# Performance work log

Measured on AMD Instinct MI355X. Metric: run time of the kernel, lower is better.

The kernel has to match this reference:

```python
import jax, jax.numpy as jnp
import numpy as np

N_NODES = 100000
N_EDGES = 1600000
F_IN, NH1, NH2, NH3, N_CLS = 128, 64, 18, 9, 10
KS = [8, 6, 4, 4]
BN_EPS = 1e-5


def setup_inputs() -> dict:
    key = jax.random.key(0)
    ks = jax.random.split(key, 32)
    inp = {
        "x": jax.random.normal(ks[0], (N_NODES, F_IN), dtype=jnp.float32),
        "edge_index": jax.random.randint(ks[1], (2, N_EDGES), 0, N_NODES, dtype=jnp.int32),
    }
    dims = [(F_IN, NH1), (NH1, NH2), (NH2, NH3), (NH3, N_CLS)]
    for i, ((din, dout), K) in enumerate(zip(dims, KS), start=1):
        scale = 1.0 / np.sqrt(din * K)
        inp[f"W{i}"] = jax.random.normal(ks[2 * i], (K, din, dout), dtype=jnp.float32) * scale
        inp[f"b{i}"] = jnp.zeros((dout,), dtype=jnp.float32)
    for i, d in enumerate([NH1, NH2, NH3], start=1):
        inp[f"bn{i}_g"] = jnp.ones((d,), dtype=jnp.float32)
        inp[f"bn{i}_b"] = jnp.zeros((d,), dtype=jnp.float32)
        inp[f"bn{i}_m"] = jnp.zeros((d,), dtype=jnp.float32)
        inp[f"bn{i}_v"] = jnp.ones((d,), dtype=jnp.float32)
    return inp


def _cheb_conv(x, W, b, src, dst, w_norm, n_nodes):
    # PyG ChebConv with lambda_max=2: L_hat = -D^{-1/2} A D^{-1/2}
    def prop(t):  # L_hat @ t via edge scatter
        return jax.ops.segment_sum(w_norm[:, None] * t[src], dst, num_segments=n_nodes)

    K = W.shape[0]
    Tx0 = x
    out = Tx0 @ W[0]
    Tx1 = prop(Tx0)
    out = out + Tx1 @ W[1]
    for k in range(2, K):
        Tx2 = 2.0 * prop(Tx1) - Tx0
        out = out + Tx2 @ W[k]
        Tx0, Tx1 = Tx1, Tx2
    return out + b


def _bn_eval(x, g, b, m, v):
    return (x - m) * (g * jax.lax.rsqrt(v + BN_EPS)) + b


def reference(x, edge_index, W1, b1, W2, b2, W3, b3, W4, b4,
              bn1_g, bn1_b, bn1_m, bn1_v,
              bn2_g, bn2_b, bn2_m, bn2_v,
              bn3_g, bn3_b, bn3_m, bn3_v):
    n = x.shape[0]
    src, dst = edge_index[0], edge_index[1]
    ones = jnp.ones((src.shape[0],), dtype=x.dtype)
    deg = jax.ops.segment_sum(ones, dst, num_segments=n)
    dinv = jnp.where(deg > 0, jax.lax.rsqrt(jnp.maximum(deg, 1.0)), 0.0)
    w_norm = -dinv[src] * dinv[dst]

    h = jax.nn.relu(_bn_eval(_cheb_conv(x, W1, b1, src, dst, w_norm, n), bn1_g, bn1_b, bn1_m, bn1_v))
    h = jax.nn.relu(_bn_eval(_cheb_conv(h, W2, b2, src, dst, w_norm, n), bn2_g, bn2_b, bn2_m, bn2_v))
    h = jax.nn.relu(_bn_eval(_cheb_conv(h, W3, b3, src, dst, w_norm, n), bn3_g, bn3_b, bn3_m, bn3_v))
    return _cheb_conv(h, W4, b4, src, dst, w_norm, n)
```

## Files before the change

kernel.cpp:

```cpp
#include <hip/hip_runtime.h>

#define NN 100000
#define NE 1600000
#define BN_EPS 1e-5f

#define BSH 7
#define BSZ (1 << BSH)
#define NBUCK 782
#define NC 192
#define CE 8334

typedef _Float16 half1;
typedef _Float16 half4 __attribute__((ext_vector_type(4)));
typedef _Float16 h8 __attribute__((ext_vector_type(8)));
typedef float f4 __attribute__((ext_vector_type(4)));
typedef float f8 __attribute__((ext_vector_type(8)));

static inline int divup(int a, int b) { return (a + b - 1) / b; }

__device__ __forceinline__ float wsrc(unsigned int q) {
    unsigned int dg = q >> 17;
    return dg ? rsqrtf((float)dg) : 0.f;
}


__global__ void hist2_kernel(const int* __restrict__ dst, int* __restrict__ deg,
                             int* __restrict__ hist_g) {
    __shared__ int h[NBUCK];
    int c = blockIdx.x;
    for (int i = threadIdx.x; i < NBUCK; i += blockDim.x) h[i] = 0;
    __syncthreads();
    int e0 = c * CE, e1 = min(e0 + CE, NE);
    for (int e = e0 + threadIdx.x; e < e1; e += blockDim.x) {
        int d = dst[e];
        atomicAdd(&deg[d], 1);
        atomicAdd(&h[d >> BSH], 1);
    }
    __syncthreads();
    for (int i = threadIdx.x; i < NBUCK; i += blockDim.x) hist_g[c * NBUCK + i] = h[i];
}

__global__ void blksum_kernel(const int* __restrict__ deg, int* __restrict__ blk, int n) {
    __shared__ int red[256];
    int t = threadIdx.x;
    int base = blockIdx.x * 1024 + t * 4;
    int s = 0;
#pragma unroll
    for (int i = 0; i < 4; ++i) {
        int idx = base + i;
        if (idx < n) s += deg[idx];
    }
    red[t] = s;
    __syncthreads();
    for (int off = 128; off > 0; off >>= 1) {
        if (t < off) red[t] += red[t + off];
        __syncthreads();
    }
    if (t == 0) blk[blockIdx.x] = red[0];
}

__global__ void blkscan_kernel(int* __restrict__ blk, int nb, int* __restrict__ row_ptr, int n) {
    __shared__ int sh[256];
    int t = threadIdx.x;
    int v = (t < nb) ? blk[t] : 0;
    sh[t] = v;
    __syncthreads();
    for (int off = 1; off < 256; off <<= 1) {
        int u = (t >= off) ? sh[t - off] : 0;
        __syncthreads();
        sh[t] += u;
        __syncthreads();
    }
    if (t < nb) blk[t] = (t == 0) ? 0 : sh[t - 1];
    if (t == nb - 1) row_ptr[n] = sh[t];
}

__global__ void emit_kernel(const int* __restrict__ deg, const int* __restrict__ blk,
                            int* __restrict__ row_ptr, int n) {
    __shared__ int red[256];
    int t = threadIdx.x;
    int base = blockIdx.x * 1024 + t * 4;
    int d[4];
    int s = 0;
#pragma unroll
    for (int i = 0; i < 4; ++i) {
        int idx = base + i;
        d[i] = (idx < n) ? deg[idx] : 0;
        s += d[i];
    }
    red[t] = s;
    __syncthreads();
    for (int off = 1; off < 256; off <<= 1) {
        int u = (t >= off) ? red[t - off] : 0;
        __syncthreads();
        red[t] += u;
        __syncthreads();
    }
    int run = blk[blockIdx.x] + ((t == 0) ? 0 : red[t - 1]);
#pragma unroll
    for (int i = 0; i < 4; ++i) {
        int idx = base + i;
        if (idx < n) { row_ptr[idx] = run; run += d[i]; }
    }
}

__global__ void bucketoff_kernel(const int* __restrict__ row_ptr, const int* __restrict__ hist_g,
                                 int* __restrict__ off_g) {
    int b = blockIdx.x * blockDim.x + threadIdx.x;
    if (b >= NBUCK) return;
    int run = row_ptr[b << BSH];
#pragma unroll 4
    for (int c = 0; c < NC; ++c) {
        off_g[c * NBUCK + b] = run;
        run += hist_g[c * NBUCK + b];
    }
}

__global__ void binscatter_kernel(const int* __restrict__ src, const int* __restrict__ dst,
                                  const int* __restrict__ deg, const int* __restrict__ off_g,
                                  int2* __restrict__ tmp) {
    __shared__ int off_l[NBUCK];
    int myx = blockIdx.x & 7;
    int c = blockIdx.x >> 3;
    for (int i = threadIdx.x; i < NBUCK; i += blockDim.x)
        off_l[i] = ((i & 7) == myx) ? off_g[c * NBUCK + i] : 0;
    __syncthreads();
    int e0 = c * CE, e1 = min(e0 + CE, NE);
    for (int e = e0 + threadIdx.x; e < e1; e += blockDim.x) {
        int d = dst[e];
        int b = d >> BSH;
        if ((b & 7) != myx) continue;
        int s = src[e];
        int dg = deg[s];
        if (dg > 32767) dg = 32767;
        int pos = atomicAdd(&off_l[b], 1);
        tmp[pos] = make_int2(s | (dg << 17), d & (BSZ - 1));
    }
}

__global__ void finalize_kernel(const int2* __restrict__ tmp, const int* __restrict__ row_ptr,
                                unsigned int* __restrict__ cw) {
    __shared__ int cnt[BSZ];
    int b = blockIdx.x;
    for (int i = threadIdx.x; i < BSZ; i += blockDim.x) cnt[i] = 0;
    __syncthreads();
    int base = b << BSH;
    int e0 = row_ptr[base];
    int e1 = row_ptr[min(base + BSZ, NN)];
    for (int e = e0 + threadIdx.x; e < e1; e += blockDim.x) {
        int2 r = tmp[e];
        int d = base + r.y;
        int k = atomicAdd(&cnt[r.y], 1);
        cw[row_ptr[d] + k] = (unsigned int)r.x;
    }
}


__global__ void cvtx_kernel(const float4* __restrict__ X, half4* __restrict__ Xh, int tot4) {
    int i = blockIdx.x * blockDim.x + threadIdx.x;
    if (i >= tot4) return;
    float4 v = X[i];
    half4 h;
    h.x = (half1)v.x; h.y = (half1)v.y; h.z = (half1)v.z; h.w = (half1)v.w;
    Xh[i] = h;
}

__global__ void transw_kernel(const float* __restrict__ W, half1* __restrict__ Wt) {
    int i = blockIdx.x * blockDim.x + threadIdx.x;
    if (i >= 512 * 128) return;
    int kd = i >> 9;
    int og = i & 511;
    int k = og >> 6, o = og & 63;
    Wt[(size_t)og * 128 + kd] = (half1)W[((size_t)k * 128 + kd) * 64 + o];
}

__global__ void padw_kernel(const float* __restrict__ src, float* __restrict__ dst,
                            int K, int dins, int douts, int dind, int doutd) {
    int i = blockIdx.x * blockDim.x + threadIdx.x;
    int tot = K * dind * doutd;
    if (i >= tot) return;
    int o = i % doutd;
    int r = i / doutd;
    int dd = r % dind;
    int k = r / dind;
    dst[i] = (dd < dins && o < douts) ? src[((size_t)k * dins + dd) * douts + o] : 0.f;
}

__global__ void proph8_kernel(const h8* __restrict__ feat, const h8* __restrict__ sub,
                              const h8* __restrict__ add, h8* __restrict__ outh,
                              f8* __restrict__ outf,
                              const int* __restrict__ row_ptr, const unsigned int* __restrict__ cw,
                              int n, float scale, int has_sub, int bnrelu,
                              const float* __restrict__ bn_g, const float* __restrict__ bn_b,
                              const float* __restrict__ bn_m, const float* __restrict__ bn_v) {
    int idx = blockIdx.x * blockDim.x + threadIdx.x;
    if (idx >= n * 8) return;
    int nd = idx >> 3;
    int f = idx & 7;
    int e0 = row_ptr[nd], e1 = row_ptr[nd + 1];
    f8 a0 = {0.f, 0.f, 0.f, 0.f, 0.f, 0.f, 0.f, 0.f}, a1 = a0, a2 = a0, a3 = a0;
    int e = e0;
    for (; e + 4 <= e1; e += 4) {
        unsigned int q0 = cw[e], q1 = cw[e + 1], q2 = cw[e + 2], q3 = cw[e + 3];
        f8 v0 = __builtin_convertvector(feat[(size_t)(q0 & 0x1FFFFu) * 8 + f], f8);
        f8 v1 = __builtin_convertvector(feat[(size_t)(q1 & 0x1FFFFu) * 8 + f], f8);
        f8 v2 = __builtin_convertvector(feat[(size_t)(q2 & 0x1FFFFu) * 8 + f], f8);
        f8 v3 = __builtin_convertvector(feat[(size_t)(q3 & 0x1FFFFu) * 8 + f], f8);
        a0 += wsrc(q0) * v0;
        a1 += wsrc(q1) * v1;
        a2 += wsrc(q2) * v2;
        a3 += wsrc(q3) * v3;
    }
    for (; e < e1; ++e) {
        unsigned int q = cw[e];
        a0 += wsrc(q) * __builtin_convertvector(feat[(size_t)(q & 0x1FFFFu) * 8 + f], f8);
    }
    int degd = e1 - e0;
    float ms = (degd > 0) ? -scale * rsqrtf((float)degd) : 0.f;
    f8 r = ((a0 + a1) + (a2 + a3)) * ms;
    if (has_sub) r -= __builtin_convertvector(sub[idx], f8);
    r += __builtin_convertvector(add[idx], f8);
    if (bnrelu) {
#pragma unroll
        for (int c = 0; c < 8; ++c) {
            int o = f * 8 + c;
            float sc = bn_g[o] * rsqrtf(bn_v[o] + BN_EPS);
            r[c] = fmaxf(fmaf(r[c] - bn_m[o], sc, bn_b[o]), 0.f);
        }
    }
    if (outf) {
        outf[idx] = r;
    } else {
        outh[idx] = __builtin_convertvector(r, h8);
    }
}

__global__ void proph_kernel(const half4* __restrict__ feat, const half4* __restrict__ sub,
                             const half4* __restrict__ add, half4* __restrict__ outh,
                             f4* __restrict__ outf,
                             const int* __restrict__ row_ptr, const unsigned int* __restrict__ cw,
                             int n, int dim4, float scale, int has_sub,
                             int bnrelu, int used,
                             const float* __restrict__ bn_g, const float* __restrict__ bn_b,
                             const float* __restrict__ bn_m, const float* __restrict__ bn_v) {
    int idx = blockIdx.x * blockDim.x + threadIdx.x;
    if (idx >= n * dim4) return;
    int nd = idx / dim4;
    int f = idx - nd * dim4;
    int e0 = row_ptr[nd], e1 = row_ptr[nd + 1];
    f4 a0 = {0.f, 0.f, 0.f, 0.f}, a1 = a0, a2 = a0, a3 = a0;
    int e = e0;
    for (; e + 4 <= e1; e += 4) {
        unsigned int q0 = cw[e], q1 = cw[e + 1], q2 = cw[e + 2], q3 = cw[e + 3];
        f4 v0 = __builtin_convertvector(feat[(size_t)(q0 & 0x1FFFFu) * dim4 + f], f4);
        f4 v1 = __builtin_convertvector(feat[(size_t)(q1 & 0x1FFFFu) * dim4 + f], f4);
        f4 v2 = __builtin_convertvector(feat[(size_t)(q2 & 0x1FFFFu) * dim4 + f], f4);
        f4 v3 = __builtin_convertvector(feat[(size_t)(q3 & 0x1FFFFu) * dim4 + f], f4);
        a0 += wsrc(q0) * v0;
        a1 += wsrc(q1) * v1;
        a2 += wsrc(q2) * v2;
        a3 += wsrc(q3) * v3;
    }
    for (; e < e1; ++e) {
        unsigned int q = cw[e];
        a0 += wsrc(q) * __builtin_convertvector(feat[(size_t)(q & 0x1FFFFu) * dim4 + f], f4);
    }
    int degd = e1 - e0;
    float ms = (degd > 0) ? -scale * rsqrtf((float)degd) : 0.f;
    f4 r = ((a0 + a1) + (a2 + a3)) * ms;
    if (has_sub) r -= __builtin_convertvector(sub[idx], f4);
    r += __builtin_convertvector(add[idx], f4);
    if (bnrelu) {
#pragma unroll
        for (int c = 0; c < 4; ++c) {
            int o = f * 4 + c;
            if (o < used) {
                float sc = bn_g[o] * rsqrtf(bn_v[o] + BN_EPS);
                r[c] = fmaxf(fmaf(r[c] - bn_m[o], sc, bn_b[o]), 0.f);
            } else r[c] = 0.f;
        }
    }
    if (outf) {
        outf[idx] = r;
    } else {
        half4 h;
        h.x = (half1)r.x; h.y = (half1)r.y; h.z = (half1)r.z; h.w = (half1)r.w;
        outh[idx] = h;
    }
}

__global__ void propl_kernel(const half4* __restrict__ feat, const half4* __restrict__ sub,
                             const half4* __restrict__ add, float* __restrict__ out,
                             const int* __restrict__ row_ptr, const unsigned int* __restrict__ cw,
                             int n) {
    int idx = blockIdx.x * blockDim.x + threadIdx.x;
    if (idx >= n * 3) return;
    int nd = idx / 3;
    int f = idx - nd * 3;
    int e0 = row_ptr[nd], e1 = row_ptr[nd + 1];
    f4 a0 = {0.f, 0.f, 0.f, 0.f}, a1 = a0, a2 = a0, a3 = a0;
    int e = e0;
    for (; e + 4 <= e1; e += 4) {
        unsigned int q0 = cw[e], q1 = cw[e + 1], q2 = cw[e + 2], q3 = cw[e + 3];
        a0 += wsrc(q0) * __builtin_convertvector(feat[(size_t)(q0 & 0x1FFFFu) * 3 + f], f4);
        a1 += wsrc(q1) * __builtin_convertvector(feat[(size_t)(q1 & 0x1FFFFu) * 3 + f], f4);
        a2 += wsrc(q2) * __builtin_convertvector(feat[(size_t)(q2 & 0x1FFFFu) * 3 + f], f4);
        a3 += wsrc(q3) * __builtin_convertvector(feat[(size_t)(q3 & 0x1FFFFu) * 3 + f], f4);
    }
    for (; e < e1; ++e) {
        unsigned int q = cw[e];
        a0 += wsrc(q) * __builtin_convertvector(feat[(size_t)(q & 0x1FFFFu) * 3 + f], f4);
    }
    int degd = e1 - e0;
    float ms = (degd > 0) ? -rsqrtf((float)degd) : 0.f;
    f4 r = ((a0 + a1) + (a2 + a3)) * ms;
    r -= __builtin_convertvector(sub[idx], f4);
    r += __builtin_convertvector(add[idx], f4);
    int o = f * 4;
    float* orow = out + (size_t)nd * 10;
    if (o + 0 < 10) orow[o + 0] = r.x;
    if (o + 1 < 10) orow[o + 1] = r.y;
    if (o + 2 < 10) orow[o + 2] = r.z;
    if (o + 3 < 10) orow[o + 3] = r.w;
}

__global__ __launch_bounds__(256) void gemm_mfma_kernel(
        const half1* __restrict__ Xh, const half1* __restrict__ Wt,
        const float* __restrict__ bias, half1* __restrict__ CB, int n) {
    int lane = threadIdx.x & 63;
    int wave = threadIdx.x >> 6;
    int m16 = lane & 15;
    int quad = lane >> 4;
    int ks = blockIdx.y * 4 + wave;
    int ntile = blockIdx.x * 64;

    f4 acc[4][4];
#pragma unroll
    for (int nt = 0; nt < 4; ++nt)
#pragma unroll
        for (int i = 0; i < 4; ++i) acc[nt][i] = (f4){0.f, 0.f, 0.f, 0.f};

#pragma unroll
    for (int kc = 0; kc < 4; ++kc) {
        int koff = kc * 32 + quad * 8;
        h8 a[4];
#pragma unroll
        for (int i = 0; i < 4; ++i)
            a[i] = *(const h8*)(Wt + (size_t)(ks * 64 + i * 16 + m16) * 128 + koff);
        h8 b[4];
#pragma unroll
        for (int nt = 0; nt < 4; ++nt) {
            int node = min(ntile + nt * 16 + m16, n - 1);
            b[nt] = *(const h8*)(Xh + (size_t)node * 128 + koff);
        }
#pragma unroll
        for (int nt = 0; nt < 4; ++nt)
#pragma unroll
            for (int i = 0; i < 4; ++i)
                acc[nt][i] = __builtin_amdgcn_mfma_f32_16x16x32_f16(a[i], b[nt], acc[nt][i], 0, 0, 0);
    }

#pragma unroll
    for (int nt = 0; nt < 4; ++nt) {
        int node = ntile + nt * 16 + m16;
        if (node < n) {
#pragma unroll
            for (int i = 0; i < 4; ++i) {
                int ob = i * 16 + quad * 4;
                f4 v = acc[nt][i];
                if (ks == 0) {
                    const f4 b4 = *(const f4*)(bias + ob);
                    v += b4;
                }
                half4 h;
                h.x = (half1)v[0]; h.y = (half1)v[1]; h.z = (half1)v[2]; h.w = (half1)v[3];
                *(half4*)(CB + ((size_t)ks * n + node) * 64 + ob) = h;
            }
        }
    }
}

template <int KK, int DIN4, int NACC>
__global__ void gemm_smallw_kernel(const float* __restrict__ X, const float* __restrict__ Wp,
                                   const float* __restrict__ bias, int dout,
                                   half4* __restrict__ CB, int n) {
    int lane = threadIdx.x & 63;
    int k = __builtin_amdgcn_readfirstlane((int)(threadIdx.x >> 6));
    int node0 = blockIdx.x * 64 + lane;
    int node = min(node0, n - 1);
    f4 acc[NACC];
#pragma unroll
    for (int i = 0; i < NACC; ++i) {
        f4 v = {0.f, 0.f, 0.f, 0.f};
        if (k == 0 && bias) {
#pragma unroll
            for (int c = 0; c < 4; ++c) {
                int o = i * 4 + c;
                v[c] = (o < dout) ? bias[o] : 0.f;
            }
        }
        acc[i] = v;
    }
    const f4* Xr = (const f4*)(X + (size_t)node * (DIN4 * 4));
    const f4* Wk = (const f4*)(Wp + (size_t)k * (DIN4 * 4) * (NACC * 4));
    for (int d4 = 0; d4 < DIN4; ++d4) {
        f4 xv = Xr[d4];
#pragma unroll
        for (int j = 0; j < 4; ++j) {
            float xs = xv[j];
#pragma unroll
            for (int i = 0; i < NACC; ++i)
                acc[i] += xs * Wk[(d4 * 4 + j) * NACC + i];
        }
    }
    if (node0 < n) {
        size_t base = ((size_t)k * n + node) * NACC;
#pragma unroll
        for (int i = 0; i < NACC; ++i) {
            half4 h;
            h.x = (half1)acc[i].x; h.y = (half1)acc[i].y;
            h.z = (half1)acc[i].z; h.w = (half1)acc[i].w;
            CB[base + i] = h;
        }
    }
}


extern "C" void kernel_launch(void* const* d_in, const int* in_sizes, int n_in,
                              void* d_out, int out_size, void* d_ws, size_t ws_size,
                              hipStream_t stream) {
    const float* x  = (const float*)d_in[0];
    const int*   ei = (const int*)d_in[1];
    const float* Wl[4] = {(const float*)d_in[2], (const float*)d_in[4],
                          (const float*)d_in[6], (const float*)d_in[8]};
    const float* bl[4] = {(const float*)d_in[3], (const float*)d_in[5],
                          (const float*)d_in[7], (const float*)d_in[9]};
    const float* bn[3][4];
    for (int l = 0; l < 3; ++l)
        for (int j = 0; j < 4; ++j)
            bn[l][j] = (const float*)d_in[10 + 4 * l + j];

    char* ws = (char*)d_ws;
    size_t off = 0;
    auto alloc = [&](size_t bytes) -> void* {
        void* p = (void*)(ws + off);
        off = (off + bytes + 255) & ~(size_t)255;
        return p;
    };
    int*   deg     = (int*)alloc(NN * 4);
    int*   row_ptr = (int*)alloc((NN + 1) * 4);
    int*   blks    = (int*)alloc(128 * 4);
    unsigned int* cw = (unsigned int*)alloc((size_t)NE * 4);
    half1* CB1h    = (half1*)alloc((size_t)8 * NN * 64 * 2);
    half1* CBsh    = (half1*)alloc((size_t)6 * NN * 20 * 2);
    half1* S0      = (half1*)alloc((size_t)NN * 64 * 2);
    half1* S1      = (half1*)alloc((size_t)NN * 64 * 2);
    half1* S2      = (half1*)alloc((size_t)NN * 64 * 2);
    float* H1f     = (float*)alloc((size_t)NN * 64 * 4);
    float* H2f     = (float*)alloc((size_t)NN * 20 * 4);
    float* H3f     = (float*)alloc((size_t)NN * 12 * 4);
    float* Wp2     = (float*)alloc((size_t)6 * 64 * 20 * 4);
    float* Wp3     = (float*)alloc((size_t)4 * 20 * 12 * 4);
    float* Wp4     = (float*)alloc((size_t)4 * 12 * 12 * 4);
    half1* Xh      = (half1*)alloc((size_t)NN * 128 * 2);
    half1* Wt1     = (half1*)alloc((size_t)512 * 128 * 2);

    int2* tmp    = (int2*)CB1h;
    int*  hist_g = (int*)((char*)CB1h + (16u << 20));
    int*  off_g  = hist_g + NC * NBUCK;

    const int* srcp = ei;
    const int* dstp = ei + NE;
    const int nscan = divup(NN, 1024);
    const int NB = divup(NN, 64);

    hipMemsetAsync(deg, 0, NN * 4, stream);
    hist2_kernel<<<NC, 256, 0, stream>>>(dstp, deg, hist_g);
    blksum_kernel<<<nscan, 256, 0, stream>>>(deg, blks, NN);
    blkscan_kernel<<<1, 256, 0, stream>>>(blks, nscan, row_ptr, NN);
    emit_kernel<<<nscan, 256, 0, stream>>>(deg, blks, row_ptr, NN);
    bucketoff_kernel<<<divup(NBUCK, 256), 256, 0, stream>>>(row_ptr, hist_g, off_g);
    binscatter_kernel<<<NC * 8, 256, 0, stream>>>(srcp, dstp, deg, off_g, tmp);
    finalize_kernel<<<NBUCK, 256, 0, stream>>>(tmp, row_ptr, cw);

    cvtx_kernel<<<divup(NN * 32, 256), 256, 0, stream>>>((const float4*)x, (half4*)Xh, NN * 32);
    transw_kernel<<<divup(512 * 128, 256), 256, 0, stream>>>(Wl[0], Wt1);
    padw_kernel<<<divup(6 * 64 * 20, 256), 256, 0, stream>>>(Wl[1], Wp2, 6, 64, 18, 64, 20);
    padw_kernel<<<divup(4 * 20 * 12, 256), 256, 0, stream>>>(Wl[2], Wp3, 4, 18, 9, 20, 12);
    padw_kernel<<<divup(4 * 12 * 12, 256), 256, 0, stream>>>(Wl[3], Wp4, 4, 9, 10, 12, 12);

    auto prop1 = [&](const half1* feat, const half1* sub, const half1* add,
                     half1* outh, float* outf, float scale, int bnrelu,
                     const float* g, const float* bb, const float* m, const float* v) {
        proph8_kernel<<<divup(NN * 8, 256), 256, 0, stream>>>(
            (const h8*)feat, (const h8*)sub, (const h8*)add,
            (h8*)outh, (f8*)outf, row_ptr, cw, NN, scale,
            sub != nullptr, bnrelu, g, bb, m, v);
    };
    auto prop = [&](const half1* feat, const half1* sub, const half1* add,
                    half1* outh, float* outf, int dim4, float scale,
                    int bnrelu, int used, const float* g, const float* bb,
                    const float* m, const float* v) {
        proph_kernel<<<divup(NN * dim4, 256), 256, 0, stream>>>(
            (const half4*)feat, (const half4*)sub, (const half4*)add,
            (half4*)outh, (f4*)outf, row_ptr, cw, NN, dim4, scale,
            sub != nullptr, bnrelu, used, g, bb, m, v);
    };

    gemm_mfma_kernel<<<dim3(NB, 2), 256, 0, stream>>>(Xh, Wt1, bl[0], CB1h, NN);
    {
        auto C = [&](int k) { return (const half1*)(CB1h + (size_t)k * NN * 64); };
        prop1(C(7), nullptr, C(6), S0, nullptr, 2.f, 0, 0, 0, 0, 0);
        prop1(S0, C(7), C(5), S1, nullptr, 2.f, 0, 0, 0, 0, 0);
        prop1(S1, S0, C(4), S2, nullptr, 2.f, 0, 0, 0, 0, 0);
        prop1(S2, S1, C(3), S0, nullptr, 2.f, 0, 0, 0, 0, 0);
        prop1(S0, S2, C(2), S1, nullptr, 2.f, 0, 0, 0, 0, 0);
        prop1(S1, S0, C(1), S2, nullptr, 2.f, 0, 0, 0, 0, 0);
        prop1(S2, S1, C(0), nullptr, H1f, 1.f, 1,
              bn[0][0], bn[0][1], bn[0][2], bn[0][3]);
    }

    gemm_smallw_kernel<6, 16, 5><<<NB, 384, 0, stream>>>(H1f, Wp2, bl[1], 18,
                                                         (half4*)CBsh, NN);
    {
        auto C = [&](int k) { return (const half1*)(CBsh + (size_t)k * NN * 20); };
        prop(C(5), nullptr, C(4), S0, nullptr, 5, 2.f, 0, 18, 0, 0, 0, 0);
        prop(S0, C(5), C(3), S1, nullptr, 5, 2.f, 0, 18, 0, 0, 0, 0);
        prop(S1, S0, C(2), S2, nullptr, 5, 2.f, 0, 18, 0, 0, 0, 0);
        prop(S2, S1, C(1), S0, nullptr, 5, 2.f, 0, 18, 0, 0, 0, 0);
        prop(S0, S2, C(0), nullptr, H2f, 5, 1.f, 1, 18,
             bn[1][0], bn[1][1], bn[1][2], bn[1][3]);
    }

    gemm_smallw_kernel<4, 5, 3><<<NB, 256, 0, stream>>>(H2f, Wp3, bl[2], 9,
                                                        (half4*)CBsh, NN);
    {
        auto C = [&](int k) { return (const half1*)(CBsh + (size_t)k * NN * 12); };
        prop(C(3), nullptr, C(2), S0, nullptr, 3, 2.f, 0, 9, 0, 0, 0, 0);
        prop(S0, C(3), C(1), S1, nullptr, 3, 2.f, 0, 9, 0, 0, 0, 0);
        prop(S1, S0, C(0), nullptr, H3f, 3, 1.f, 1, 9,
             bn[2][0], bn[2][1], bn[2][2], bn[2][3]);
    }

    gemm_smallw_kernel<4, 3, 3><<<NB, 256, 0, stream>>>(H3f, Wp4, bl[3], 10,
                                                        (half4*)CBsh, NN);
    {
        auto C = [&](int k) { return (const half1*)(CBsh + (size_t)k * NN * 12); };
        prop(C(3), nullptr, C(2), S0, nullptr, 3, 2.f, 0, 10, 0, 0, 0, 0);
        prop(S0, C(3), C(1), S1, nullptr, 3, 2.f, 0, 10, 0, 0, 0, 0);
        propl_kernel<<<divup(NN * 3, 256), 256, 0, stream>>>(
            (const half4*)S1, (const half4*)S0, (const half4*)CBsh,
            (float*)d_out, row_ptr, cw, NN);
    }
}
```

Baseline: 856.2 us.

## Rebuild CSR construction via bucket scan, widen gather unroll, tune GEMM launch

Replaces the degree-atomic histogram and three-kernel node scan with a bucket-level scan. Per-node offsets and degrees are now computed inside finalize from local counts, and a separate packdeg pass folds source degrees into the edge words. It also adds an 8-way unrolled gather loop in the 64-wide propagation kernel, nontemporal loads of the add operand and nontemporal stores of the GEMM output. The first GEMM moves from a 2D grid of 256-thread blocks to 512-thread blocks covering all 8 k-slices. These changes aim to cut global atomics, kernel launches and memory traffic in preprocessing and to raise memory-level parallelism in the gathers, at the cost of one extra pass over the edge array and more register pressure.

```diff
diff --git a/kernel.cpp b/kernel.cpp
--- a/kernel.cpp
+++ b/kernel.cpp
@@ -24,91 +24,42 @@
 }
 
 
-__global__ void hist2_kernel(const int* __restrict__ dst, int* __restrict__ deg,
-                             int* __restrict__ hist_g) {
+__global__ void histb_kernel(const int* __restrict__ dst, int* __restrict__ hist_g) {
     __shared__ int h[NBUCK];
     int c = blockIdx.x;
     for (int i = threadIdx.x; i < NBUCK; i += blockDim.x) h[i] = 0;
     __syncthreads();
     int e0 = c * CE, e1 = min(e0 + CE, NE);
-    for (int e = e0 + threadIdx.x; e < e1; e += blockDim.x) {
-        int d = dst[e];
-        atomicAdd(&deg[d], 1);
-        atomicAdd(&h[d >> BSH], 1);
-    }
+    for (int e = e0 + threadIdx.x; e < e1; e += blockDim.x)
+        atomicAdd(&h[dst[e] >> BSH], 1);
     __syncthreads();
     for (int i = threadIdx.x; i < NBUCK; i += blockDim.x) hist_g[c * NBUCK + i] = h[i];
 }
 
-__global__ void blksum_kernel(const int* __restrict__ deg, int* __restrict__ blk, int n) {
-    __shared__ int red[256];
+__global__ void bscan1_kernel(const int* __restrict__ hist_g, int* __restrict__ bucket_start,
+                              int* __restrict__ row_ptr) {
+    __shared__ int sh[1024];
     int t = threadIdx.x;
-    int base = blockIdx.x * 1024 + t * 4;
-    int s = 0;
-#pragma unroll
-    for (int i = 0; i < 4; ++i) {
-        int idx = base + i;
-        if (idx < n) s += deg[idx];
-    }
-    red[t] = s;
-    __syncthreads();
-    for (int off = 128; off > 0; off >>= 1) {
-        if (t < off) red[t] += red[t + off];
+    int tot = 0;
+    if (t < NBUCK)
+        for (int c = 0; c < NC; ++c) tot += hist_g[c * NBUCK + t];
+    sh[t] = (t < NBUCK) ? tot : 0;
+    __syncthreads();
+    for (int off = 1; off < 1024; off <<= 1) {
+        int v = (t >= off) ? sh[t - off] : 0;
         __syncthreads();
-    }
-    if (t == 0) blk[blockIdx.x] = red[0];
-}
-
-__global__ void blkscan_kernel(int* __restrict__ blk, int nb, int* __restrict__ row_ptr, int n) {
-    __shared__ int sh[256];
-    int t = threadIdx.x;
-    int v = (t < nb) ? blk[t] : 0;
-    sh[t] = v;
-    __syncthreads();
-    for (int off = 1; off < 256; off <<= 1) {
-        int u = (t >= off) ? sh[t - off] : 0;
+        sh[t] += v;
         __syncthreads();
-        sh[t] += u;
-        __syncthreads();
-    }
-    if (t < nb) blk[t] = (t == 0) ? 0 : sh[t - 1];
-    if (t == nb - 1) row_ptr[n] = sh[t];
-}
-
-__global__ void emit_kernel(const int* __restrict__ deg, const int* __restrict__ blk,
-                            int* __restrict__ row_ptr, int n) {
-    __shared__ int red[256];
-    int t = threadIdx.x;
-    int base = blockIdx.x * 1024 + t * 4;
-    int d[4];
-    int s = 0;
-#pragma unroll
-    for (int i = 0; i < 4; ++i) {
-        int idx = base + i;
-        d[i] = (idx < n) ? deg[idx] : 0;
-        s += d[i];
-    }
-    red[t] = s;
-    __syncthreads();
-    for (int off = 1; off < 256; off <<= 1) {
-        int u = (t >= off) ? red[t - off] : 0;
-        __syncthreads();
-        red[t] += u;
-        __syncthreads();
-    }
-    int run = blk[blockIdx.x] + ((t == 0) ? 0 : red[t - 1]);
-#pragma unroll
-    for (int i = 0; i < 4; ++i) {
-        int idx = base + i;
-        if (idx < n) { row_ptr[idx] = run; run += d[i]; }
-    }
-}
-
-__global__ void bucketoff_kernel(const int* __restrict__ row_ptr, const int* __restrict__ hist_g,
-                                 int* __restrict__ off_g) {
+    }
+    if (t < NBUCK) bucket_start[t] = sh[t] - tot;
+    if (t == 0) { bucket_start[NBUCK] = NE; row_ptr[NN] = NE; }
+}
+
+__global__ void boff_kernel(const int* __restrict__ bucket_start, const int* __restrict__ hist_g,
+                            int* __restrict__ off_g) {
     int b = blockIdx.x * blockDim.x + threadIdx.x;
     if (b >= NBUCK) return;
-    int run = row_ptr[b << BSH];
+    int run = bucket_start[b];
 #pragma unroll 4
     for (int c = 0; c < NC; ++c) {
         off_g[c * NBUCK + b] = run;
@@ -117,8 +68,7 @@
 }
 
 __global__ void binscatter_kernel(const int* __restrict__ src, const int* __restrict__ dst,
-                                  const int* __restrict__ deg, const int* __restrict__ off_g,
-                                  int2* __restrict__ tmp) {
+                                  const int* __restrict__ off_g, unsigned int* __restrict__ tmp) {
     __shared__ int off_l[NBUCK];
     int myx = blockIdx.x & 7;
     int c = blockIdx.x >> 3;
@@ -131,28 +81,52 @@
         int b = d >> BSH;
         if ((b & 7) != myx) continue;
         int s = src[e];
-        int dg = deg[s];
-        if (dg > 32767) dg = 32767;
         int pos = atomicAdd(&off_l[b], 1);
-        tmp[pos] = make_int2(s | (dg << 17), d & (BSZ - 1));
-    }
-}
-
-__global__ void finalize_kernel(const int2* __restrict__ tmp, const int* __restrict__ row_ptr,
+        tmp[pos] = (unsigned int)s | ((unsigned int)(d & (BSZ - 1)) << 25);
+    }
+}
+
+__global__ void finalize_kernel(const unsigned int* __restrict__ tmp,
+                                const int* __restrict__ bucket_start,
+                                int* __restrict__ row_ptr, int* __restrict__ deg,
                                 unsigned int* __restrict__ cw) {
-    __shared__ int cnt[BSZ];
-    int b = blockIdx.x;
-    for (int i = threadIdx.x; i < BSZ; i += blockDim.x) cnt[i] = 0;
-    __syncthreads();
-    int base = b << BSH;
-    int e0 = row_ptr[base];
-    int e1 = row_ptr[min(base + BSZ, NN)];
-    for (int e = e0 + threadIdx.x; e < e1; e += blockDim.x) {
-        int2 r = tmp[e];
-        int d = base + r.y;
-        int k = atomicAdd(&cnt[r.y], 1);
-        cw[row_ptr[d] + k] = (unsigned int)r.x;
-    }
+    __shared__ int cnt[BSZ], sc[BSZ], cur[BSZ];
+    int b = blockIdx.x, t = threadIdx.x;
+    int e0 = bucket_start[b], e1 = bucket_start[b + 1];
+    if (t < BSZ) cnt[t] = 0;
+    __syncthreads();
+    for (int e = e0 + t; e < e1; e += blockDim.x) atomicAdd(&cnt[tmp[e] >> 25], 1);
+    __syncthreads();
+    if (t < BSZ) sc[t] = cnt[t];
+    __syncthreads();
+    for (int off = 1; off < BSZ; off <<= 1) {
+        int v = (t >= off && t < BSZ) ? sc[t - off] : 0;
+        __syncthreads();
+        if (t < BSZ) sc[t] += v;
+        __syncthreads();
+    }
+    if (t < BSZ) {
+        int p = e0 + sc[t] - cnt[t];
+        cur[t] = p;
+        int nd = (b << BSH) + t;
+        if (nd < NN) { row_ptr[nd] = p; deg[nd] = cnt[t]; }
+    }
+    __syncthreads();
+    for (int e = e0 + t; e < e1; e += blockDim.x) {
+        unsigned int r = tmp[e];
+        int ld = r >> 25;
+        int k = atomicAdd(&cur[ld], 1);
+        cw[k] = r & 0x1FFFFu;
+    }
+}
+
+__global__ void packdeg_kernel(unsigned int* __restrict__ cw, const int* __restrict__ deg) {
+    int e = blockIdx.x * blockDim.x + threadIdx.x;
+    if (e >= NE) return;
+    unsigned int q = cw[e];
+    int dg = deg[q];
+    if (dg > 32767) dg = 32767;
+    cw[e] = q | ((unsigned int)dg << 17);
 }
 
 
@@ -200,6 +174,26 @@
     int e0 = row_ptr[nd], e1 = row_ptr[nd + 1];
     f8 a0 = {0.f, 0.f, 0.f, 0.f, 0.f, 0.f, 0.f, 0.f}, a1 = a0, a2 = a0, a3 = a0;
     int e = e0;
+    for (; e + 8 <= e1; e += 8) {
+        unsigned int q0 = cw[e], q1 = cw[e + 1], q2 = cw[e + 2], q3 = cw[e + 3];
+        unsigned int q4 = cw[e + 4], q5 = cw[e + 5], q6 = cw[e + 6], q7 = cw[e + 7];
+        f8 v0 = __builtin_convertvector(feat[(size_t)(q0 & 0x1FFFFu) * 8 + f], f8);
+        f8 v1 = __builtin_convertvector(feat[(size_t)(q1 & 0x1FFFFu) * 8 + f], f8);
+        f8 v2 = __builtin_convertvector(feat[(size_t)(q2 & 0x1FFFFu) * 8 + f], f8);
+        f8 v3 = __builtin_convertvector(feat[(size_t)(q3 & 0x1FFFFu) * 8 + f], f8);
+        f8 v4 = __builtin_convertvector(feat[(size_t)(q4 & 0x1FFFFu) * 8 + f], f8);
+        f8 v5 = __builtin_convertvector(feat[(size_t)(q5 & 0x1FFFFu) * 8 + f], f8);
+        f8 v6 = __builtin_convertvector(feat[(size_t)(q6 & 0x1FFFFu) * 8 + f], f8);
+        f8 v7 = __builtin_convertvector(feat[(size_t)(q7 & 0x1FFFFu) * 8 + f], f8);
+        a0 += wsrc(q0) * v0;
+        a1 += wsrc(q1) * v1;
+        a2 += wsrc(q2) * v2;
+        a3 += wsrc(q3) * v3;
+        a0 += wsrc(q4) * v4;
+        a1 += wsrc(q5) * v5;
+        a2 += wsrc(q6) * v6;
+        a3 += wsrc(q7) * v7;
+    }
     for (; e + 4 <= e1; e += 4) {
         unsigned int q0 = cw[e], q1 = cw[e + 1], q2 = cw[e + 2], q3 = cw[e + 3];
         f8 v0 = __builtin_convertvector(feat[(size_t)(q0 & 0x1FFFFu) * 8 + f], f8);
@@ -219,7 +213,7 @@
     float ms = (degd > 0) ? -scale * rsqrtf((float)degd) : 0.f;
     f8 r = ((a0 + a1) + (a2 + a3)) * ms;
     if (has_sub) r -= __builtin_convertvector(sub[idx], f8);
-    r += __builtin_convertvector(add[idx], f8);
+    r += __builtin_convertvector(__builtin_nontemporal_load(&add[idx]), f8);
     if (bnrelu) {
 #pragma unroll
         for (int c = 0; c < 8; ++c) {
@@ -269,7 +263,7 @@
     float ms = (degd > 0) ? -scale * rsqrtf((float)degd) : 0.f;
     f4 r = ((a0 + a1) + (a2 + a3)) * ms;
     if (has_sub) r -= __builtin_convertvector(sub[idx], f4);
-    r += __builtin_convertvector(add[idx], f4);
+    r += __builtin_convertvector(__builtin_nontemporal_load(&add[idx]), f4);
     if (bnrelu) {
 #pragma unroll
         for (int c = 0; c < 4; ++c) {
@@ -324,14 +318,13 @@
     if (o + 3 < 10) orow[o + 3] = r.w;
 }
 
-__global__ __launch_bounds__(256) void gemm_mfma_kernel(
+__global__ __launch_bounds__(512) void gemm_mfma_kernel(
         const half1* __restrict__ Xh, const half1* __restrict__ Wt,
         const float* __restrict__ bias, half1* __restrict__ CB, int n) {
     int lane = threadIdx.x & 63;
-    int wave = threadIdx.x >> 6;
+    int ks = threadIdx.x >> 6;
     int m16 = lane & 15;
     int quad = lane >> 4;
-    int ks = blockIdx.y * 4 + wave;
     int ntile = blockIdx.x * 64;
 
     f4 acc[4][4];
@@ -374,7 +367,7 @@
                 }
                 half4 h;
                 h.x = (half1)v[0]; h.y = (half1)v[1]; h.z = (half1)v[2]; h.w = (half1)v[3];
-                *(half4*)(CB + ((size_t)ks * n + node) * 64 + ob) = h;
+                __builtin_nontemporal_store(h, (half4*)(CB + ((size_t)ks * n + node) * 64 + ob));
             }
         }
     }
@@ -447,9 +440,9 @@
         off = (off + bytes + 255) & ~(size_t)255;
         return p;
     };
-    int*   deg     = (int*)alloc(NN * 4);
-    int*   row_ptr = (int*)alloc((NN + 1) * 4);
-    int*   blks    = (int*)alloc(128 * 4);
+    int*   deg      = (int*)alloc(NN * 4);
+    int*   row_ptr  = (int*)alloc((NN + 1) * 4);
+    int*   bstart   = (int*)alloc((NBUCK + 1) * 4);
     unsigned int* cw = (unsigned int*)alloc((size_t)NE * 4);
     half1* CB1h    = (half1*)alloc((size_t)8 * NN * 64 * 2);
     half1* CBsh    = (half1*)alloc((size_t)6 * NN * 20 * 2);
@@ -465,23 +458,20 @@
     half1* Xh      = (half1*)alloc((size_t)NN * 128 * 2);
     half1* Wt1     = (half1*)alloc((size_t)512 * 128 * 2);
 
-    int2* tmp    = (int2*)CB1h;
-    int*  hist_g = (int*)((char*)CB1h + (16u << 20));
-    int*  off_g  = hist_g + NC * NBUCK;
+    unsigned int* tmp = (unsigned int*)CB1h;
+    int* hist_g = (int*)((char*)CB1h + (16u << 20));
+    int* off_g  = hist_g + NC * NBUCK;
 
     const int* srcp = ei;
     const int* dstp = ei + NE;
-    const int nscan = divup(NN, 1024);
     const int NB = divup(NN, 64);
 
-    hipMemsetAsync(deg, 0, NN * 4, stream);
-    hist2_kernel<<<NC, 256, 0, stream>>>(dstp, deg, hist_g);
-    blksum_kernel<<<nscan, 256, 0, stream>>>(deg, blks, NN);
-    blkscan_kernel<<<1, 256, 0, stream>>>(blks, nscan, row_ptr, NN);
-    emit_kernel<<<nscan, 256, 0, stream>>>(deg, blks, row_ptr, NN);
-    bucketoff_kernel<<<divup(NBUCK, 256), 256, 0, stream>>>(row_ptr, hist_g, off_g);
-    binscatter_kernel<<<NC * 8, 256, 0, stream>>>(srcp, dstp, deg, off_g, tmp);
-    finalize_kernel<<<NBUCK, 256, 0, stream>>>(tmp, row_ptr, cw);
+    histb_kernel<<<NC, 256, 0, stream>>>(dstp, hist_g);
+    bscan1_kernel<<<1, 1024, 0, stream>>>(hist_g, bstart, row_ptr);
+    boff_kernel<<<divup(NBUCK, 256), 256, 0, stream>>>(bstart, hist_g, off_g);
+    binscatter_kernel<<<NC * 8, 256, 0, stream>>>(srcp, dstp, off_g, tmp);
+    finalize_kernel<<<NBUCK, 256, 0, stream>>>(tmp, bstart, row_ptr, deg, cw);
+    packdeg_kernel<<<divup(NE, 256), 256, 0, stream>>>(cw, deg);
 
     cvtx_kernel<<<divup(NN * 32, 256), 256, 0, stream>>>((const float4*)x, (half4*)Xh, NN * 32);
     transw_kernel<<<divup(512 * 128, 256), 256, 0, stream>>>(Wl[0], Wt1);
@@ -507,7 +497,7 @@
             sub != nullptr, bnrelu, used, g, bb, m, v);
     };
 
-    gemm_mfma_kernel<<<dim3(NB, 2), 256, 0, stream>>>(Xh, Wt1, bl[0], CB1h, NN);
+    gemm_mfma_kernel<<<NB, 512, 0, stream>>>(Xh, Wt1, bl[0], CB1h, NN);
     {
         auto C = [&](int k) { return (const half1*)(CB1h + (size_t)k * NN * 64); };
         prop1(C(7), nullptr, C(6), S0, nullptr, 2.f, 0, 0, 0, 0, 0);
```

New measurement: 825.0 us. 1.04x faster.
